# Optimization experiments

Measured on AMD Instinct MI355X. Metric: run time of the kernel, lower is better.

Reference implementation:

```python
import jax, jax.numpy as jnp
import numpy as np

# module config (init_kwargs)
AH, AW = 14, 14            # aligned_height, aligned_width
SCALE = 0.25               # spatial_scale
RATIO = 2                  # sampling_ratio
SHIFT = 0.0                # spatial_shift (added in feature-map coords)
HALF_PART = 0              # 0 = full box
ROI_SCALE = 1.0            # box rescale about its center


def setup_inputs() -> dict:
    key = jax.random.key(0)
    kf, kb, kx, ky, kw, kh = jax.random.split(key, 6)
    B, C, H, W = 2, 256, 200, 272
    N = 256
    features = jax.random.normal(kf, (B, C, H, W), dtype=jnp.float32)
    img_h, img_w = H / SCALE, W / SCALE
    bidx = jax.random.randint(kb, (N,), 0, B).astype(jnp.float32)
    x1 = jax.random.uniform(kx, (N,)) * (img_w * 0.6)
    y1 = jax.random.uniform(ky, (N,)) * (img_h * 0.6)
    bw = 32.0 + jax.random.uniform(kw, (N,)) * (img_w * 0.35)
    bh = 32.0 + jax.random.uniform(kh, (N,)) * (img_h * 0.35)
    rois = jnp.stack([bidx, x1, y1, x1 + bw, y1 + bh], axis=1).astype(jnp.float32)
    return {"features": features, "rois": rois}


def _lin_idx(coord, size):
    # bilinear index/weight prep with RoIAlign boundary rules
    valid = (coord > -1.0) & (coord < float(size))
    c = jnp.clip(coord, 0.0, float(size - 1))
    lo = jnp.floor(c)
    hi = jnp.minimum(lo + 1.0, float(size - 1))
    frac = c - lo
    return lo.astype(jnp.int32), hi.astype(jnp.int32), frac, valid.astype(coord.dtype)


def _roi_mask_align(features, rois):
    B, C, H, W = features.shape
    N = rois.shape[0]
    PH, PW, r = AH + 1, AW + 1, RATIO
    b = rois[:, 0].astype(jnp.int32)
    # to feature-map coords, with roi_scale about the box center and spatial_shift
    x1, y1, x2, y2 = (rois[:, 1] * SCALE, rois[:, 2] * SCALE,
                      rois[:, 3] * SCALE, rois[:, 4] * SCALE)
    cx, cy = 0.5 * (x1 + x2), 0.5 * (y1 + y2)
    hw, hh = 0.5 * (x2 - x1) * ROI_SCALE, 0.5 * (y2 - y1) * ROI_SCALE
    x1, x2 = cx - hw + SHIFT, cx + hw + SHIFT
    y1, y2 = cy - hh + SHIFT, cy + hh + SHIFT
    roi_w = jnp.maximum(x2 - x1, 1.0)
    roi_h = jnp.maximum(y2 - y1, 1.0)
    bin_w = roi_w / PW
    bin_h = roi_h / PH
    # sample coords, separable: sx [N, PW*r], sy [N, PH*r]
    ix = jnp.arange(PW * r, dtype=jnp.float32)
    iy = jnp.arange(PH * r, dtype=jnp.float32)
    sx = x1[:, None] + (ix[None, :] + 0.5) * (bin_w[:, None] / r)
    sy = y1[:, None] + (iy[None, :] + 0.5) * (bin_h[:, None] / r)
    y_lo, y_hi, fy, vy = _lin_idx(sy, H)
    x_lo, x_hi, fx, vx = _lin_idx(sx, W)
    featsT = jnp.transpose(features, (0, 2, 3, 1))  # [B,H,W,C]
    bb = b[:, None, None]
    gather = lambda yi, xi: featsT[bb, yi[:, :, None], xi[:, None, :]]  # [N,Sy,Sx,C]
    wy0, wy1 = 1.0 - fy, fy
    wx0, wx1 = 1.0 - fx, fx
    val = (gather(y_lo, x_lo) * (wy0[:, :, None] * wx0[:, None, :])[..., None]
           + gather(y_lo, x_hi) * (wy0[:, :, None] * wx1[:, None, :])[..., None]
           + gather(y_hi, x_lo) * (wy1[:, :, None] * wx0[:, None, :])[..., None]
           + gather(y_hi, x_hi) * (wy1[:, :, None] * wx1[:, None, :])[..., None])
    val = val * (vy[:, :, None] * vx[:, None, :])[..., None]
    # average the r*r samples per bin -> [N, PH, PW, C]
    val = val.reshape(N, PH, r, PW, r, C).mean(axis=(2, 4))
    return jnp.transpose(val, (0, 3, 1, 2))  # [N, C, PH, PW]


def reference(features, rois):
    x = _roi_mask_align(features, rois)  # [N, C, AH+1, AW+1]
    # avg_pool2d(kernel=2, stride=1)
    out = 0.25 * (x[..., :-1, :-1] + x[..., 1:, :-1]
                  + x[..., :-1, 1:] + x[..., 1:, 1:])
    return out  # [N, C, AH, AW]
```

## Files before the change

kernel.cpp:

```cpp
#include <hip/hip_runtime.h>


#define AH_ 14
#define AW_ 14
#define NS_ 30
#define C_  256
#define H_  200
#define W_  272
#define CPB 4
#define VS_ 33
#define HS_ 15

__global__ __launch_bounds__(256)
void roi_mask_align_avg_kernel(const float* __restrict__ feat,
                               const float* __restrict__ rois,
                               float* __restrict__ out) {
    __shared__ float V[CPB][NS_ * VS_];
    __shared__ float Hs[CPB][NS_ * HS_];

    const int p   = blockIdx.x;
    const int xcd = p & 7;
    const int q   = p >> 3;
    const int n   = q & 255;
    const int cgi = q >> 8;
    const int cg  = cgi * 8 + xcd;
    const int c0  = cg * CPB;

    const int tid  = threadIdx.x;
    const int wave = tid >> 6;
    const int lane = tid & 63;
    const int ix   = lane & 31;
    const int half = lane >> 5;

    const float r0f = rois[n * 5 + 0];
    const float x1s = rois[n * 5 + 1] * 0.25f;
    const float y1s = rois[n * 5 + 2] * 0.25f;
    const float x2s = rois[n * 5 + 3] * 0.25f;
    const float y2s = rois[n * 5 + 4] * 0.25f;
    const int   b   = (int)r0f;

    const float cx = 0.5f * (x1s + x2s), cy = 0.5f * (y1s + y2s);
    const float hw = 0.5f * (x2s - x1s), hh = 0.5f * (y2s - y1s);
    const float x1 = cx - hw, x2 = cx + hw;
    const float y1 = cy - hh, y2 = cy + hh;
    const float roi_w = fmaxf(x2 - x1, 1.0f);
    const float roi_h = fmaxf(y2 - y1, 1.0f);
    const float sub_w = roi_w * (1.0f / 15.0f) * 0.5f;
    const float sub_h = roi_h * (1.0f / 15.0f) * 0.5f;

    const float sx  = x1 + ((float)ix + 0.5f) * sub_w;
    const bool  vx_ = (sx > -1.0f) && (sx < (float)W_);
    const float ccx = fminf(fmaxf(sx, 0.0f), (float)(W_ - 1));
    const float lox = floorf(ccx);
    const int   xl  = (int)lox;
    const int   xh  = min(xl + 1, W_ - 1);
    const float fx  = ccx - lox;
    const float vmx = vx_ ? 1.0f : 0.0f;
    const float wx0 = (1.0f - fx) * vmx;
    const float wx1 = fx * vmx;

    const int c = c0 + wave;
    const float* __restrict__ fp = feat + ((size_t)b * C_ + c) * (size_t)(H_ * W_);
    float* __restrict__ Vw = V[wave];

    #pragma unroll 5
    for (int ps = 0; ps < 15; ++ps) {
        const int   iy  = 2 * ps + half;
        const float sy  = y1 + ((float)iy + 0.5f) * sub_h;
        const bool  vy_ = (sy > -1.0f) && (sy < (float)H_);
        const float ccy = fminf(fmaxf(sy, 0.0f), (float)(H_ - 1));
        const float loy = floorf(ccy);
        const int   yl  = (int)loy;
        const int   yh  = min(yl + 1, H_ - 1);
        const float fy  = ccy - loy;
        const float vmy = vy_ ? 1.0f : 0.0f;
        const float wy0 = (1.0f - fy) * vmy;
        const float wy1 = fy * vmy;

        const float* r0p = fp + yl * W_;
        const float* r1p = fp + yh * W_;
        const float v = r0p[xl] * (wy0 * wx0) + r0p[xh] * (wy0 * wx1)
                      + r1p[xl] * (wy1 * wx0) + r1p[xh] * (wy1 * wx1);
        if (ix < NS_) Vw[iy * VS_ + ix] = v;
    }
    __syncthreads();

    float* __restrict__ Hw = Hs[wave];
    for (int o = lane; o < NS_ * AW_; o += 64) {
        const int iy = o / AW_;
        const int aw = o - iy * AW_;
        const float* vr = Vw + iy * VS_ + 2 * aw;
        Hw[iy * HS_ + aw] = vr[0] + vr[1] + vr[2] + vr[3];
    }
    __syncthreads();

    float* __restrict__ op = out + ((size_t)n * C_ + c) * (AH_ * AW_);
    for (int o = lane; o < AH_ * AW_; o += 64) {
        const int ah = o / AW_;
        const int aw = o - ah * AW_;
        const float* hr = Hw + (2 * ah) * HS_ + aw;
        op[o] = (hr[0] + hr[HS_] + hr[2 * HS_] + hr[3 * HS_]) * (1.0f / 16.0f);
    }
}

extern "C" void kernel_launch(void* const* d_in, const int* in_sizes, int n_in,
                              void* d_out, int out_size, void* d_ws, size_t ws_size,
                              hipStream_t stream) {
    const float* feat = (const float*)d_in[0];
    const float* rois = (const float*)d_in[1];
    float* out = (float*)d_out;
    const int grid = 256 * (C_ / CPB);
    roi_mask_align_avg_kernel<<<grid, 256, 0, stream>>>(feat, rois, out);
}
```

Before: 258.6 us.

## Process four channels per wave in registers, replacing LDS pooling with shuffles

Each wave now handles four channels, with the two 32-lane halves taking different channels and each lane looping over all 30 sample rows. Row offsets are made wave-uniform through readfirstlane. The horizontal 2x2 sample averaging and the stride-1 avg-pool are done with lane shuffles and a running register carry across row pairs, so shared memory and both __syncthreads are gone. The grid shrinks to 16 blocks per ROI and drops the XCD-aware block remap. This trades LDS traffic and barriers for more loads in flight per thread and higher register pressure from the fully unrolled loop.

Measured after the change: 286.0 us. 1.11x slower.

```diff
diff --git a/kernel.cpp b/kernel.cpp
--- a/kernel.cpp
+++ b/kernel.cpp
@@ -1,36 +1,28 @@
 #include <hip/hip_runtime.h>
 
 
-#define AH_ 14
-#define AW_ 14
-#define NS_ 30
-#define C_  256
-#define H_  200
-#define W_  272
-#define CPB 4
-#define VS_ 33
-#define HS_ 15
+#define AH_  14
+#define AW_  14
+#define C_   256
+#define H_   200
+#define W_   272
+#define HW_  (H_ * W_)
+#define CPW  4
+#define CPB  (4 * CPW)
+#define NPAIR 15
 
 __global__ __launch_bounds__(256)
 void roi_mask_align_avg_kernel(const float* __restrict__ feat,
                                const float* __restrict__ rois,
                                float* __restrict__ out) {
-    __shared__ float V[CPB][NS_ * VS_];
-    __shared__ float Hs[CPB][NS_ * HS_];
-
-    const int p   = blockIdx.x;
-    const int xcd = p & 7;
-    const int q   = p >> 3;
-    const int n   = q & 255;
-    const int cgi = q >> 8;
-    const int cg  = cgi * 8 + xcd;
-    const int c0  = cg * CPB;
-
+    const int p    = blockIdx.x;
+    const int n    = p >> 4;
+    const int cg   = p & 15;
     const int tid  = threadIdx.x;
     const int wave = tid >> 6;
     const int lane = tid & 63;
+    const int half = lane >> 5;
     const int ix   = lane & 31;
-    const int half = lane >> 5;
 
     const float r0f = rois[n * 5 + 0];
     const float x1s = rois[n * 5 + 1] * 0.25f;
@@ -49,7 +41,7 @@
     const float sub_h = roi_h * (1.0f / 15.0f) * 0.5f;
 
     const float sx  = x1 + ((float)ix + 0.5f) * sub_w;
-    const bool  vx_ = (sx > -1.0f) && (sx < (float)W_);
+    const bool  vx_ = (sx > -1.0f) && (sx < (float)W_) && (ix < 30);
     const float ccx = fminf(fmaxf(sx, 0.0f), (float)(W_ - 1));
     const float lox = floorf(ccx);
     const int   xl  = (int)lox;
@@ -59,47 +51,66 @@
     const float wx0 = (1.0f - fx) * vmx;
     const float wx1 = fx * vmx;
 
-    const int c = c0 + wave;
-    const float* __restrict__ fp = feat + ((size_t)b * C_ + c) * (size_t)(H_ * W_);
-    float* __restrict__ Vw = V[wave];
+    const int cA = cg * CPB + wave * CPW;
+    const float* __restrict__ bpA = feat + ((size_t)b * C_ + cA) * (size_t)HW_;
+    const float* __restrict__ bpB = bpA + 2 * HW_;
+    const int vx0 = half * HW_ + xl;
+    const int vx1 = half * HW_ + xh;
 
-    #pragma unroll 5
-    for (int ps = 0; ps < 15; ++ps) {
-        const int   iy  = 2 * ps + half;
-        const float sy  = y1 + ((float)iy + 0.5f) * sub_h;
-        const bool  vy_ = (sy > -1.0f) && (sy < (float)H_);
-        const float ccy = fminf(fmaxf(sy, 0.0f), (float)(H_ - 1));
-        const float loy = floorf(ccy);
-        const int   yl  = (int)loy;
-        const int   yh  = min(yl + 1, H_ - 1);
-        const float fy  = ccy - loy;
-        const float vmy = vy_ ? 1.0f : 0.0f;
-        const float wy0 = (1.0f - fy) * vmy;
-        const float wy1 = fy * vmy;
+    float* __restrict__ opA = out + ((size_t)n * C_ + cA) * (AH_ * AW_);
+    const int  aw   = ix >> 1;
+    const int  so   = half * (AH_ * AW_) + aw;
+    const bool emit = ((lane & 1) == 0) && (aw < AW_);
 
-        const float* r0p = fp + yl * W_;
-        const float* r1p = fp + yh * W_;
-        const float v = r0p[xl] * (wy0 * wx0) + r0p[xh] * (wy0 * wx1)
-                      + r1p[xl] * (wy1 * wx0) + r1p[xh] * (wy1 * wx1);
-        if (ix < NS_) Vw[iy * VS_ + ix] = v;
-    }
-    __syncthreads();
+    float prevSA = 0.0f, prevSB = 0.0f;
 
-    float* __restrict__ Hw = Hs[wave];
-    for (int o = lane; o < NS_ * AW_; o += 64) {
-        const int iy = o / AW_;
-        const int aw = o - iy * AW_;
-        const float* vr = Vw + iy * VS_ + 2 * aw;
-        Hw[iy * HS_ + aw] = vr[0] + vr[1] + vr[2] + vr[3];
-    }
-    __syncthreads();
+    #pragma unroll
+    for (int k = 0; k < NPAIR; ++k) {
+        float PA = 0.0f, PB = 0.0f;
+        #pragma unroll
+        for (int r = 0; r < 2; ++r) {
+            const int iy = 2 * k + r;
+            const float sy  = y1 + ((float)iy + 0.5f) * sub_h;
+            const bool  vy_ = (sy > -1.0f) && (sy < (float)H_);
+            const float ccy = fminf(fmaxf(sy, 0.0f), (float)(H_ - 1));
+            const float loy = floorf(ccy);
+            const int   yl  = (int)loy;
+            const int   yh  = min(yl + 1, H_ - 1);
+            const float fy  = ccy - loy;
+            const float vmy = vy_ ? 1.0f : 0.0f;
+            const float wy0 = (1.0f - fy) * vmy;
+            const float wy1 = fy * vmy;
 
-    float* __restrict__ op = out + ((size_t)n * C_ + c) * (AH_ * AW_);
-    for (int o = lane; o < AH_ * AW_; o += 64) {
-        const int ah = o / AW_;
-        const int aw = o - ah * AW_;
-        const float* hr = Hw + (2 * ah) * HS_ + aw;
-        op[o] = (hr[0] + hr[HS_] + hr[2 * HS_] + hr[3 * HS_]) * (1.0f / 16.0f);
+            const int ro0 = __builtin_amdgcn_readfirstlane(yl * W_);
+            const int ro1 = __builtin_amdgcn_readfirstlane(yh * W_);
+            const float* __restrict__ rA0 = bpA + ro0;
+            const float* __restrict__ rA1 = bpA + ro1;
+            const float* __restrict__ rB0 = bpB + ro0;
+            const float* __restrict__ rB1 = bpB + ro1;
+
+            const float w00 = wy0 * wx0, w01 = wy0 * wx1;
+            const float w10 = wy1 * wx0, w11 = wy1 * wx1;
+
+            const float a00 = rA0[vx0], a01 = rA0[vx1];
+            const float a10 = rA1[vx0], a11 = rA1[vx1];
+            const float c00 = rB0[vx0], c01 = rB0[vx1];
+            const float c10 = rB1[vx0], c11 = rB1[vx1];
+
+            const float vA = a00 * w00 + a01 * w01 + a10 * w10 + a11 * w11;
+            const float vB = c00 * w00 + c01 * w01 + c10 * w10 + c11 * w11;
+            PA += vA;
+            PB += vB;
+        }
+        const float tA = PA + __shfl_xor(PA, 1, 64);
+        const float uA = tA + __shfl_down(tA, 2, 64);
+        const float tB = PB + __shfl_xor(PB, 1, 64);
+        const float uB = tB + __shfl_down(tB, 2, 64);
+        if (k > 0 && emit) {
+            opA[so + (k - 1) * AW_]                    = (prevSA + uA) * 0.0625f;
+            opA[so + (k - 1) * AW_ + 2 * (AH_ * AW_)]  = (prevSB + uB) * 0.0625f;
+        }
+        prevSA = uA;
+        prevSB = uB;
     }
 }
 
```
